# Performance work log

Measured on AMD Instinct MI355X. Metric: run time of the kernel, lower is better.

## Reference

```python
import jax, jax.numpy as jnp
import numpy as np

TAU = 2.0
V_TH = 1.0
V_RESET = 0.0


def setup_inputs() -> dict:
    key = jax.random.key(0)
    k1, k2 = jax.random.split(key)
    T, N, C, H, W = 16, 8, 64, 64, 64
    x_seq = jax.random.normal(k1, (T, N, C, H, W), dtype=jnp.float32)
    conv_weight = jax.random.normal(k2, (C, C, 3, 3), dtype=jnp.float32) * 0.05
    return {"x_seq": x_seq, "conv_weight": conv_weight}


def _conv2d(x, w):
    # x: (B, C, H, W), w: (Cout, Cin, 3, 3), padding=1, no bias
    return jax.lax.conv_general_dilated(
        x, w, window_strides=(1, 1), padding=((1, 1), (1, 1)),
        dimension_numbers=("NCHW", "OIHW", "NCHW"))


def _lif_scan(z_seq):
    # z_seq: (T, N, C, H, W); LIF: decay_input=True, hard reset to V_RESET.
    def step(v, x):
        # charge: v = v + (x - (v - v_reset)) / tau
        v = v + (x - (v - V_RESET)) / TAU
        s = (v >= V_TH).astype(v.dtype)
        # hard reset: v = (1 - s) * v + s * v_reset
        v = (1.0 - s) * v + s * V_RESET
        return v, s

    v0 = jnp.full(z_seq.shape[1:], V_RESET, dtype=z_seq.dtype)
    _, spikes = jax.lax.scan(step, v0, z_seq)
    return spikes


def reference(x_seq, conv_weight):
    T, N = x_seq.shape[:2]
    z = _conv2d(x_seq.reshape(T * N, *x_seq.shape[2:]), conv_weight)
    z = z.reshape(T, N, *z.shape[1:])
    return _lif_scan(z)
```

## Files before the change

kernel.cpp:

```cpp
#include <hip/hip_runtime.h>


namespace {
constexpr int T = 16, N = 8, C = 64, H = 64, W = 64;
constexpr int HW   = H * W;
constexpr int CHW  = C * HW;
constexpr int NCHW = N * CHW;
constexpr int NWT  = C * C * 9;
constexpr int PSTR = 68;
}

__global__ void wtr_kernel(const float* __restrict__ w, float* __restrict__ wt2) {
    int i = blockIdx.x * 256 + threadIdx.x;
    if (i >= NWT) return;
    int tap  = i % 9;
    int rem  = i / 9;
    int ci   = rem % 64;
    int cout = rem / 64;
    wt2[(tap * 64 + ci) * 64 + cout] = w[i];
}

__global__ __launch_bounds__(256, 5) void conv_kernel(
    const float* __restrict__ x,
    const float* __restrict__ wt2,
    float*       __restrict__ zo)
{
#pragma clang fp contract(off)
    __shared__ float xs[100 * PSTR];

    const int tid  = threadIdx.x;
    const int wave = __builtin_amdgcn_readfirstlane(tid >> 6);
    const int lane = tid & 63;
    const int px = lane & 7;
    const int py = lane >> 3;
    const int c0 = wave << 4;

    const int bid  = blockIdx.x;
    const int t    = bid >> 9;
    const int r    = bid & 511;
    const int n    = r >> 6;
    const int tile = r & 63;
    const int th0 = (tile >> 3) << 3;
    const int tw0 = (tile & 7) << 3;

    const float* xt = x + (size_t)(t * N + n) * CHW;

#pragma unroll
    for (int it = 0; it < 25; ++it) {
        int j  = tid + it * 256;
        int ci = j / 100;
        int rr = j - ci * 100;
        int dy = rr / 10;
        int dx = rr - dy * 10;
        int hh = th0 - 1 + dy;
        int ww = tw0 - 1 + dx;
        float val = 0.0f;
        if ((unsigned)hh < (unsigned)H && (unsigned)ww < (unsigned)W)
            val = xt[ci * HW + hh * W + ww];
        xs[rr * PSTR + ci] = val;
    }
    __syncthreads();

    float acc[16];
#pragma unroll
    for (int i = 0; i < 16; ++i) acc[i] = 0.0f;

    for (int tap = 0; tap < 9; ++tap) {
        const int ky = tap / 3, kx = tap - 3 * ky;
        const int pos = (py + ky) * 10 + (px + kx);
        const float4* xp = (const float4*)xs + pos * (PSTR / 4);
        const float* wtap = wt2 + tap * 4096 + c0;
#pragma unroll 2
        for (int cib = 0; cib < 16; ++cib) {
            const float4 xv = xp[cib];
            const float* wp = wtap + cib * 256;
#pragma unroll
            for (int cc = 0; cc < 16; ++cc)
                acc[cc] = fmaf(wp[cc], xv.x, acc[cc]);
#pragma unroll
            for (int cc = 0; cc < 16; ++cc)
                acc[cc] = fmaf(wp[64 + cc], xv.y, acc[cc]);
#pragma unroll
            for (int cc = 0; cc < 16; ++cc)
                acc[cc] = fmaf(wp[128 + cc], xv.z, acc[cc]);
#pragma unroll
            for (int cc = 0; cc < 16; ++cc)
                acc[cc] = fmaf(wp[192 + cc], xv.w, acc[cc]);
        }
    }

    float* zt = zo + (size_t)(t * N + n) * CHW;
    const int pbase = (th0 + py) * W + (tw0 + px);
#pragma unroll
    for (int cc = 0; cc < 16; ++cc)
        zt[(c0 + cc) * HW + pbase] = acc[cc];
}

__global__ void lif_kernel(float* __restrict__ zo) {
#pragma clang fp contract(off)
    const int gid = blockIdx.x * 256 + threadIdx.x;
    float v = 0.0f;
#pragma unroll
    for (int t = 0; t < T; ++t) {
        float* p = zo + (size_t)t * NCHW + gid;
        float z = *p;
        float d = z - v;
        float h = d * 0.5f;
        v = v + h;
        float s;
        if (v >= 1.0f) { s = 1.0f; v = 0.0f; } else { s = 0.0f; }
        *p = s;
    }
}

extern "C" void kernel_launch(void* const* d_in, const int* in_sizes, int n_in,
                              void* d_out, int out_size, void* d_ws, size_t ws_size,
                              hipStream_t stream) {
    const float* x = (const float*)d_in[0];
    const float* w = (const float*)d_in[1];
    if (n_in >= 2 && in_sizes[0] < in_sizes[1]) {
        const float* tmp = x; x = w; w = tmp;
    }
    float* out = (float*)d_out;
    float* wt2 = (float*)d_ws;

    wtr_kernel<<<(NWT + 255) / 256, 256, 0, stream>>>(w, wt2);
    conv_kernel<<<T * N * 64, 256, 0, stream>>>(x, wt2, out);
    lif_kernel<<<NCHW / 256, 256, 0, stream>>>(out);
}
```

Measured before the change: 673.9 us.

## Widen conv tiles to 8x16 with 512 threads, swizzle LDS, vectorize LIF

```diff
diff --git a/kernel.cpp b/kernel.cpp
--- a/kernel.cpp
+++ b/kernel.cpp
@@ -8,6 +8,10 @@
 constexpr int NCHW = N * CHW;
 constexpr int NWT  = C * C * 9;
 constexpr int PSTR = 68;
+constexpr int TH = 8, TW = 16;
+constexpr int PH = TH + 2;
+constexpr int PW = TW + 2;
+constexpr int NPOS = PH * PW;
 }
 
 __global__ void wtr_kernel(const float* __restrict__ w, float* __restrict__ wt2) {
@@ -20,44 +24,51 @@
     wt2[(tap * 64 + ci) * 64 + cout] = w[i];
 }
 
-__global__ __launch_bounds__(256, 5) void conv_kernel(
+__global__ __launch_bounds__(512, 6) void conv_kernel(
     const float* __restrict__ x,
     const float* __restrict__ wt2,
     float*       __restrict__ zo)
 {
 #pragma clang fp contract(off)
-    __shared__ float xs[100 * PSTR];
+    __shared__ float xs[NPOS * PSTR];
 
     const int tid  = threadIdx.x;
     const int wave = __builtin_amdgcn_readfirstlane(tid >> 6);
     const int lane = tid & 63;
     const int px = lane & 7;
     const int py = lane >> 3;
-    const int c0 = wave << 4;
+    const int ph8 = (wave & 1) << 3;
+    const int c0  = (wave >> 1) << 4;
 
     const int bid  = blockIdx.x;
-    const int t    = bid >> 9;
-    const int r    = bid & 511;
-    const int n    = r >> 6;
-    const int tile = r & 63;
-    const int th0 = (tile >> 3) << 3;
-    const int tw0 = (tile & 7) << 3;
+    const int t    = bid >> 8;
+    const int r    = bid & 255;
+    const int n    = r >> 5;
+    const int tile = r & 31;
+    const int th0 = (tile >> 2) << 3;
+    const int tw0 = (tile & 3) << 4;
 
     const float* xt = x + (size_t)(t * N + n) * CHW;
 
+    const int p3 = tid & 7;
+    const int c3 = (tid >> 3) & 7;
 #pragma unroll
-    for (int it = 0; it < 25; ++it) {
-        int j  = tid + it * 256;
-        int ci = j / 100;
-        int rr = j - ci * 100;
-        int dy = rr / 10;
-        int dx = rr - dy * 10;
-        int hh = th0 - 1 + dy;
-        int ww = tw0 - 1 + dx;
-        float val = 0.0f;
-        if ((unsigned)hh < (unsigned)H && (unsigned)ww < (unsigned)W)
-            val = xt[ci * HW + hh * W + ww];
-        xs[rr * PSTR + ci] = val;
+    for (int it = 0; it < 23; ++it) {
+        int rem = it * 8 + wave;
+        int cb  = rem / 23;
+        int pb  = rem - cb * 23;
+        int pos = pb * 8 + p3;
+        if (pos < NPOS) {
+            int ci = cb * 8 + c3;
+            int dy = pos / PW;
+            int dx = pos - dy * PW;
+            int hh = th0 - 1 + dy;
+            int ww = tw0 - 1 + dx;
+            float val = 0.0f;
+            if ((unsigned)hh < (unsigned)H && (unsigned)ww < (unsigned)W)
+                val = xt[ci * HW + hh * W + ww];
+            xs[pos * PSTR + ((((ci >> 2) ^ (pb & 7)) << 2) | (ci & 3))] = val;
+        }
     }
     __syncthreads();
 
@@ -67,12 +78,13 @@
 
     for (int tap = 0; tap < 9; ++tap) {
         const int ky = tap / 3, kx = tap - 3 * ky;
-        const int pos = (py + ky) * 10 + (px + kx);
+        const int pos = (py + ky) * PW + (ph8 + px + kx);
+        const int g   = (pos >> 3) & 7;
         const float4* xp = (const float4*)xs + pos * (PSTR / 4);
         const float* wtap = wt2 + tap * 4096 + c0;
-#pragma unroll 2
+#pragma unroll 4
         for (int cib = 0; cib < 16; ++cib) {
-            const float4 xv = xp[cib];
+            const float4 xv = xp[cib ^ g];
             const float* wp = wtap + cib * 256;
 #pragma unroll
             for (int cc = 0; cc < 16; ++cc)
@@ -90,7 +102,7 @@
     }
 
     float* zt = zo + (size_t)(t * N + n) * CHW;
-    const int pbase = (th0 + py) * W + (tw0 + px);
+    const int pbase = (th0 + py) * W + (tw0 + ph8 + px);
 #pragma unroll
     for (int cc = 0; cc < 16; ++cc)
         zt[(c0 + cc) * HW + pbase] = acc[cc];
@@ -99,16 +111,19 @@
 __global__ void lif_kernel(float* __restrict__ zo) {
 #pragma clang fp contract(off)
     const int gid = blockIdx.x * 256 + threadIdx.x;
-    float v = 0.0f;
+    float4 v;
+    v.x = 0.0f; v.y = 0.0f; v.z = 0.0f; v.w = 0.0f;
 #pragma unroll
     for (int t = 0; t < T; ++t) {
-        float* p = zo + (size_t)t * NCHW + gid;
-        float z = *p;
-        float d = z - v;
-        float h = d * 0.5f;
-        v = v + h;
-        float s;
-        if (v >= 1.0f) { s = 1.0f; v = 0.0f; } else { s = 0.0f; }
+        float4* p = (float4*)(zo + (size_t)t * NCHW) + gid;
+        float4 z = *p;
+        float4 s;
+#define LIF_STEP(comp) { float d = z.comp - v.comp; float hh = d * 0.5f;      \
+        v.comp = v.comp + hh;                                                  \
+        if (v.comp >= 1.0f) { s.comp = 1.0f; v.comp = 0.0f; }                  \
+        else                { s.comp = 0.0f; } }
+        LIF_STEP(x) LIF_STEP(y) LIF_STEP(z) LIF_STEP(w)
+#undef LIF_STEP
         *p = s;
     }
 }
@@ -125,6 +140,6 @@
     float* wt2 = (float*)d_ws;
 
     wtr_kernel<<<(NWT + 255) / 256, 256, 0, stream>>>(w, wt2);
-    conv_kernel<<<T * N * 64, 256, 0, stream>>>(x, wt2, out);
-    lif_kernel<<<NCHW / 256, 256, 0, stream>>>(out);
+    conv_kernel<<<T * N * 32, 512, 0, stream>>>(x, wt2, out);
+    lif_kernel<<<NCHW / 1024, 256, 0, stream>>>(out);
 }
```

Result: slower. 795.0 us (+18.0%).

## Fuse LIF scan into conv kernel with per-block time loop and swizzled LDS

Applied to the files above, without the earlier changes.

```diff
diff --git a/kernel.cpp b/kernel.cpp
--- a/kernel.cpp
+++ b/kernel.cpp
@@ -20,10 +20,10 @@
     wt2[(tap * 64 + ci) * 64 + cout] = w[i];
 }
 
-__global__ __launch_bounds__(256, 5) void conv_kernel(
+__global__ __launch_bounds__(256, 2) void fused_kernel(
     const float* __restrict__ x,
     const float* __restrict__ wt2,
-    float*       __restrict__ zo)
+    float*       __restrict__ out)
 {
 #pragma clang fp contract(off)
     __shared__ float xs[100 * PSTR];
@@ -36,80 +36,82 @@
     const int c0 = wave << 4;
 
     const int bid  = blockIdx.x;
-    const int t    = bid >> 9;
-    const int r    = bid & 511;
-    const int n    = r >> 6;
-    const int tile = r & 63;
+    const int n    = bid >> 6;
+    const int tile = bid & 63;
     const int th0 = (tile >> 3) << 3;
     const int tw0 = (tile & 7) << 3;
 
-    const float* xt = x + (size_t)(t * N + n) * CHW;
+    const float* xn = x   + (size_t)n * CHW;
+    float*       on = out + (size_t)n * CHW;
 
+    const int pbase = (th0 + py) * W + (tw0 + px);
+
+    float v[16];
 #pragma unroll
-    for (int it = 0; it < 25; ++it) {
-        int j  = tid + it * 256;
-        int ci = j / 100;
-        int rr = j - ci * 100;
-        int dy = rr / 10;
-        int dx = rr - dy * 10;
-        int hh = th0 - 1 + dy;
-        int ww = tw0 - 1 + dx;
-        float val = 0.0f;
-        if ((unsigned)hh < (unsigned)H && (unsigned)ww < (unsigned)W)
-            val = xt[ci * HW + hh * W + ww];
-        xs[rr * PSTR + ci] = val;
-    }
-    __syncthreads();
+    for (int i = 0; i < 16; ++i) v[i] = 0.0f;
 
-    float acc[16];
+#pragma unroll 1
+    for (int t = 0; t < T; ++t) {
+        const float* xt = xn + (size_t)t * NCHW;
+
+        __syncthreads();
 #pragma unroll
-    for (int i = 0; i < 16; ++i) acc[i] = 0.0f;
+        for (int it = 0; it < 25; ++it) {
+            int j  = tid + it * 256;
+            int ci = j / 100;
+            int rr = j - ci * 100;
+            int dy = rr / 10;
+            int dx = rr - dy * 10;
+            int hh = th0 - 1 + dy;
+            int ww = tw0 - 1 + dx;
+            float val = 0.0f;
+            if ((unsigned)hh < (unsigned)H && (unsigned)ww < (unsigned)W)
+                val = xt[ci * HW + hh * W + ww];
+            xs[rr * PSTR + ((((ci >> 2) ^ (dy & 7)) << 2) | (ci & 3))] = val;
+        }
+        __syncthreads();
 
-    for (int tap = 0; tap < 9; ++tap) {
-        const int ky = tap / 3, kx = tap - 3 * ky;
-        const int pos = (py + ky) * 10 + (px + kx);
-        const float4* xp = (const float4*)xs + pos * (PSTR / 4);
-        const float* wtap = wt2 + tap * 4096 + c0;
-#pragma unroll 2
-        for (int cib = 0; cib < 16; ++cib) {
-            const float4 xv = xp[cib];
-            const float* wp = wtap + cib * 256;
+        float acc[16];
 #pragma unroll
-            for (int cc = 0; cc < 16; ++cc)
-                acc[cc] = fmaf(wp[cc], xv.x, acc[cc]);
+        for (int i = 0; i < 16; ++i) acc[i] = 0.0f;
+
+        for (int tap = 0; tap < 9; ++tap) {
+            const int ky = tap / 3, kx = tap - 3 * ky;
+            const int pos = (py + ky) * 10 + (px + kx);
+            const int g   = (py + ky) & 7;
+            const float4* xp = (const float4*)xs + pos * (PSTR / 4);
+            const float* wtap = wt2 + tap * 4096 + c0;
+#pragma unroll 4
+            for (int cib = 0; cib < 16; ++cib) {
+                const float4 xv = xp[cib ^ g];
+                const float* wp = wtap + cib * 256;
 #pragma unroll
-            for (int cc = 0; cc < 16; ++cc)
-                acc[cc] = fmaf(wp[64 + cc], xv.y, acc[cc]);
+                for (int cc = 0; cc < 16; ++cc)
+                    acc[cc] = fmaf(wp[cc], xv.x, acc[cc]);
 #pragma unroll
-            for (int cc = 0; cc < 16; ++cc)
-                acc[cc] = fmaf(wp[128 + cc], xv.z, acc[cc]);
+                for (int cc = 0; cc < 16; ++cc)
+                    acc[cc] = fmaf(wp[64 + cc], xv.y, acc[cc]);
 #pragma unroll
-            for (int cc = 0; cc < 16; ++cc)
-                acc[cc] = fmaf(wp[192 + cc], xv.w, acc[cc]);
+                for (int cc = 0; cc < 16; ++cc)
+                    acc[cc] = fmaf(wp[128 + cc], xv.z, acc[cc]);
+#pragma unroll
+                for (int cc = 0; cc < 16; ++cc)
+                    acc[cc] = fmaf(wp[192 + cc], xv.w, acc[cc]);
+            }
         }
-    }
 
-    float* zt = zo + (size_t)(t * N + n) * CHW;
-    const int pbase = (th0 + py) * W + (tw0 + px);
+        float* ot = on + (size_t)t * NCHW;
 #pragma unroll
-    for (int cc = 0; cc < 16; ++cc)
-        zt[(c0 + cc) * HW + pbase] = acc[cc];
-}
-
-__global__ void lif_kernel(float* __restrict__ zo) {
-#pragma clang fp contract(off)
-    const int gid = blockIdx.x * 256 + threadIdx.x;
-    float v = 0.0f;
-#pragma unroll
-    for (int t = 0; t < T; ++t) {
-        float* p = zo + (size_t)t * NCHW + gid;
-        float z = *p;
-        float d = z - v;
-        float h = d * 0.5f;
-        v = v + h;
-        float s;
-        if (v >= 1.0f) { s = 1.0f; v = 0.0f; } else { s = 0.0f; }
-        *p = s;
+        for (int cc = 0; cc < 16; ++cc) {
+            float z = acc[cc];
+            float d = z - v[cc];
+            float h = d * 0.5f;
+            float vv = v[cc] + h;
+            float s;
+            if (vv >= 1.0f) { s = 1.0f; vv = 0.0f; } else { s = 0.0f; }
+            v[cc] = vv;
+            ot[(c0 + cc) * HW + pbase] = s;
+        }
     }
 }
 
@@ -125,6 +127,5 @@
     float* wt2 = (float*)d_ws;
 
     wtr_kernel<<<(NWT + 255) / 256, 256, 0, stream>>>(w, wt2);
-    conv_kernel<<<T * N * 64, 256, 0, stream>>>(x, wt2, out);
-    lif_kernel<<<NCHW / 256, 256, 0, stream>>>(out);
+    fused_kernel<<<N * 64, 256, 0, stream>>>(x, wt2, out);
 }
```

Measured after the change: 1.652 ms. 145% more time.
